# Kernel tuning notes

Measured on AMD Instinct MI355X. Metric: run time of the kernel, lower is better.

## Reference

```python
import jax, jax.numpy as jnp
import numpy as np
import math

DIM = 512
HEADS = 8
DH = DIM // HEADS
B, C, H, W = 2, 512, 48, 48


def setup_inputs() -> dict:
    key = jax.random.key(0)
    k1, k2, k3, k4 = jax.random.split(key, 4)
    x = jax.random.normal(k1, (B, C, H, W), dtype=jnp.float32)
    # torch Linear weights: [out_features, in_features]
    w_qkv = jax.random.normal(k2, (3 * DIM, DIM), dtype=jnp.float32) * (DIM ** -0.5)
    w_out = jax.random.normal(k3, (DIM, DIM), dtype=jnp.float32) * (DIM ** -0.5)
    b_out = jax.random.normal(k4, (DIM,), dtype=jnp.float32) * 0.01
    wavelength = jnp.asarray(0.1, dtype=jnp.float32)
    return {"x": x, "w_qkv": w_qkv, "w_out": w_out, "b_out": b_out, "wavelength": wavelength}


def reference(x, w_qkv, w_out, b_out, wavelength):
    b, c, h, w = x.shape
    n = h * w
    scale = DH ** -0.5

    x_flat = x.reshape(b, c, n).transpose(0, 2, 1)  # [B, N, C]
    qkv = jnp.einsum('bnc,dc->bnd', x_flat, w_qkv)   # [B, N, 3*DIM]
    q, k, v = jnp.split(qkv, 3, axis=-1)

    def to_heads(t):
        return t.reshape(b, n, HEADS, DH).transpose(0, 2, 1, 3)  # [B, h, N, dh]

    q, k, v = to_heads(q), to_heads(k), to_heads(v)

    dots = jnp.einsum('bhid,bhjd->bhij', q, k) * scale  # [B, h, N, N]

    # Fresnel interference bias over spatial positions
    yy, xx = jnp.meshgrid(jnp.arange(h), jnp.arange(w), indexing='ij')
    positions = jnp.stack([yy, xx], axis=-1).astype(jnp.float32).reshape(-1, 2)  # [N, 2]
    pos_diff = positions[None, :, :] - positions[:, None, :]  # [N, N, 2]
    distances = jnp.sqrt(jnp.sum(pos_diff ** 2, axis=-1) + 1e-8)  # [N, N]
    phase = 2.0 * math.pi * distances / (jnp.abs(wavelength) * h + 1e-6)
    interference = jnp.cos(phase)

    dots = dots + interference[None, None, :, :] * 0.1
    attn = jax.nn.softmax(dots, axis=-1)
    out = jnp.einsum('bhij,bhjd->bhid', attn, v)  # [B, h, N, dh]
    out = out.transpose(0, 2, 1, 3).reshape(b, n, HEADS * DH)  # [B, N, DIM]
    out = jnp.einsum('bnd,od->bno', out, w_out) + b_out
    return out.transpose(0, 2, 1).reshape(b, c, h, w)
```

## Files before the change

### kernel.cpp

```cpp
#include <hip/hip_runtime.h>
#include <math.h>

#define BB 2
#define CC 512
#define NN 2304
#define NH 8
#define DD 512
#define D3 1536
#define WIDTH 48
#define C1 0.18033688f

typedef _Float16 h8 __attribute__((ext_vector_type(8)));
typedef _Float16 h4 __attribute__((ext_vector_type(4)));
typedef _Float16 h2 __attribute__((ext_vector_type(2)));
typedef float f4 __attribute__((ext_vector_type(4)));

__device__ __forceinline__ void gload16(const void* g, void* s) {
  __builtin_amdgcn_global_load_lds(
      (const __attribute__((address_space(1))) unsigned int*)g,
      (__attribute__((address_space(3))) unsigned int*)s, 16, 0, 0);
}

__global__ __launch_bounds__(128) void btf_k(const float* __restrict__ wavp,
                                             _Float16* __restrict__ btf)
{
  const int t = threadIdx.x;
  const int qbk = blockIdx.x, ktk = blockIdx.y;
  const int w = t >> 6, quad = (t >> 4) & 3, l15 = t & 15;
  const float pc = 6.283185307179586f / (fabsf(wavp[0]) * (float)WIDTH + 1e-6f);
  _Float16* o = btf + (((size_t)qbk * 36 + ktk) * 128 + t) * 32;
#pragma unroll
  for (int g = 0; g < 4; ++g) {
    h8 v;
#pragma unroll
    for (int e = 0; e < 8; ++e) {
      const int j = g * 8 + e;
      const int nt = j >> 4, mt = (j >> 2) & 3, r = j & 3;
      const int q = qbk * 64 + w * 32 + nt * 16 + l15;
      const int k = ktk * 64 + mt * 16 + quad * 4 + r;
      const float dy = (float)(q / WIDTH) - (float)(k / WIDTH);
      const float dx = (float)(q % WIDTH) - (float)(k % WIDTH);
      const float dist = sqrtf(dy * dy + dx * dx + 1e-8f);
      v[e] = (_Float16)(0.1f * __cosf(dist * pc) * 1.44269504f);
    }
    *(h8*)(o + g * 8) = v;
  }
}

__global__ __launch_bounds__(256) void tx_k(const float* __restrict__ x,
                                            _Float16* __restrict__ xt)
{
  __shared__ float Ls[32][33];
  const int t = threadIdx.x;
  const int n0 = blockIdx.x * 32, c0 = blockIdx.y * 32, b = blockIdx.z;
#pragma unroll
  for (int p = 0; p < 4; ++p) {
    const int cl = (t >> 5) + p * 8, nl = t & 31;
    Ls[cl][nl] = x[((size_t)b * CC + c0 + cl) * NN + n0 + nl];
  }
  __syncthreads();
#pragma unroll
  for (int p = 0; p < 2; ++p) {
    const int nl = (t >> 4) + p * 16, cl = (t & 15) * 2;
    h2 v = {(_Float16)Ls[cl][nl], (_Float16)Ls[cl + 1][nl]};
    *(h2*)(xt + ((size_t)b * NN + n0 + nl) * CC + c0 + cl) = v;
  }
}

__global__ __launch_bounds__(256) void convw_k(const float* __restrict__ wq,
                                               const float* __restrict__ wo,
                                               _Float16* __restrict__ wqh,
                                               _Float16* __restrict__ woh)
{
  const int idx = blockIdx.x * 256 + threadIdx.x;
  const int NQ = (D3 * CC) / 4;
  if (idx < NQ) {
    float4 v = *(const float4*)(wq + (size_t)idx * 4);
    h4 o = {(_Float16)v.x, (_Float16)v.y, (_Float16)v.z, (_Float16)v.w};
    *(h4*)(wqh + (size_t)idx * 4) = o;
  } else {
    const int j = idx - NQ;
    float4 v = *(const float4*)(wo + (size_t)j * 4);
    h4 o = {(_Float16)v.x, (_Float16)v.y, (_Float16)v.z, (_Float16)v.w};
    *(h4*)(woh + (size_t)j * 4) = o;
  }
}

__global__ __launch_bounds__(64) void qkv_gemm_k(
    const _Float16* __restrict__ xt, const _Float16* __restrict__ wqh,
    _Float16* __restrict__ qb, _Float16* __restrict__ kb,
    _Float16* __restrict__ vb)
{
  __shared__ _Float16 Xs[2][64][32];
  __shared__ _Float16 Ws[2][64][32];
  const int t = threadIdx.x;
  const int l15 = t & 15, quad = t >> 4;
  const int n0 = blockIdx.x * 64;
  const int d0 = blockIdx.y * 64;
  const int b  = blockIdx.z;
  const bool isv = (d0 >= 2 * DD);
  const _Float16* xb = xt + (size_t)b * NN * CC;
  const int srow = t >> 2, scol = (t & 3) * 8;

  f4 acc[4][4];
#pragma unroll
  for (int mt = 0; mt < 4; ++mt)
#pragma unroll
    for (int nt = 0; nt < 4; ++nt) acc[mt][nt] = (f4)(0.f);

  auto stage = [&](int bf, int c0) {
#pragma unroll
    for (int ci = 0; ci < 4; ++ci) {
      const int row = ci * 16 + srow;
      gload16(xb + (size_t)(n0 + row) * CC + c0 + scol,
              &Xs[bf][0][0] + ci * 512);
      gload16(wqh + (size_t)(d0 + row) * CC + c0 + scol,
              &Ws[bf][0][0] + ci * 512);
    }
  };

  stage(0, 0);
  for (int i = 0; i < 16; ++i) {
    const int cur = i & 1;
    __syncthreads();
    if (i < 15) stage(cur ^ 1, (i + 1) * 32);
    h8 wfr[4], xfr[4];
#pragma unroll
    for (int mt = 0; mt < 4; ++mt)
      wfr[mt] = *(const h8*)&Ws[cur][mt * 16 + l15][quad * 8];
#pragma unroll
    for (int nt = 0; nt < 4; ++nt)
      xfr[nt] = *(const h8*)&Xs[cur][nt * 16 + l15][quad * 8];
    if (!isv) {
#pragma unroll
      for (int mt = 0; mt < 4; ++mt)
#pragma unroll
        for (int nt = 0; nt < 4; ++nt)
          acc[mt][nt] = __builtin_amdgcn_mfma_f32_16x16x32_f16(
              wfr[mt], xfr[nt], acc[mt][nt], 0, 0, 0);
    } else {
#pragma unroll
      for (int mt = 0; mt < 4; ++mt)
#pragma unroll
        for (int nt = 0; nt < 4; ++nt)
          acc[mt][nt] = __builtin_amdgcn_mfma_f32_16x16x32_f16(
              xfr[nt], wfr[mt], acc[mt][nt], 0, 0, 0);
    }
  }

  if (!isv) {
    const int which = d0 >> 9;
    _Float16* buf = which == 0 ? qb : kb;
    const int h = (d0 & 511) >> 6;
#pragma unroll
    for (int mt = 0; mt < 4; ++mt) {
      const int dh = mt * 16 + quad * 4;
#pragma unroll
      for (int nt = 0; nt < 4; ++nt) {
        const int token = n0 + nt * 16 + l15;
        h4 o = {(_Float16)acc[mt][nt][0], (_Float16)acc[mt][nt][1],
                (_Float16)acc[mt][nt][2], (_Float16)acc[mt][nt][3]};
        *(h4*)(buf + (((size_t)b * NH + h) * NN + token) * 64 + dh) = o;
      }
    }
  } else {
    const int h = (d0 - 2 * DD) >> 6;
#pragma unroll
    for (int mt = 0; mt < 4; ++mt) {
      const int dh = mt * 16 + l15;
#pragma unroll
      for (int nt = 0; nt < 4; ++nt) {
        const int token = n0 + nt * 16 + quad * 4;
        h4 o = {(_Float16)acc[mt][nt][0], (_Float16)acc[mt][nt][1],
                (_Float16)acc[mt][nt][2], (_Float16)acc[mt][nt][3]};
        *(h4*)(vb + (((size_t)b * NH + h) * 64 + dh) * NN + token) = o;
      }
    }
  }
}

__global__ __launch_bounds__(128, 3) void attn_k(
    const _Float16* __restrict__ qb, const _Float16* __restrict__ kb,
    const _Float16* __restrict__ vb, const _Float16* __restrict__ btf,
    _Float16* __restrict__ op, float* __restrict__ lp)
{
  __shared__ _Float16 Ks[64][72];
  __shared__ _Float16 Vs[64][72];
  __shared__ _Float16 Ps[2][32][72];

  const int t    = threadIdx.x;
  const int lane = t & 63;
  const int w    = t >> 6;
  const int l15  = lane & 15;
  const int quad = lane >> 4;
  const int qt = blockIdx.x >> 1;
  const int s  = blockIdx.x & 1;
  const int h = blockIdx.y, b = blockIdx.z;
  const int n0 = qt * 64;
  const size_t base = ((size_t)b * NH + h) * NN * 64;
  const _Float16* qp = qb + base;
  const _Float16* kp = kb + base;
  const _Float16* vp = vb + base;

  h8 qf[2][2];
#pragma unroll
  for (int nt = 0; nt < 2; ++nt)
#pragma unroll
    for (int ks = 0; ks < 2; ++ks)
      qf[nt][ks] = *(const h8*)(qp + (size_t)(n0 + w * 32 + nt * 16 + l15) * 64 +
                                ks * 32 + quad * 8);

  f4 oc[4][2];
#pragma unroll
  for (int mt = 0; mt < 4; ++mt)
#pragma unroll
    for (int nt = 0; nt < 2; ++nt) oc[mt][nt] = (f4)(0.f);
  float lacc[2][4] = {};

  const int srow = t >> 3, soff = (t & 7) * 8;
  const _Float16* bp = btf + (((size_t)qt * 36 + s * 18) * 128 + t) * 32;

  h8 kr[4], vr[4], br[4];
  {
    const int k0 = s * 18 * 64;
#pragma unroll
    for (int r = 0; r < 4; ++r) {
      const int row = srow + r * 16;
      kr[r] = *(const h8*)(kp + (size_t)(k0 + row) * 64 + soff);
      vr[r] = *(const h8*)(vp + (size_t)row * NN + k0 + soff);
      br[r] = *(const h8*)(bp + r * 8);
    }
  }

  for (int kt = 0; kt < 18; ++kt) {
    __syncthreads();
#pragma unroll
    for (int r = 0; r < 4; ++r) {
      const int row = srow + r * 16;
      *(h8*)&Ks[row][soff] = kr[r];
      *(h8*)&Vs[row][soff] = vr[r];
    }
    h8 bfr[4];
#pragma unroll
    for (int r = 0; r < 4; ++r) bfr[r] = br[r];
    __syncthreads();

    if (kt < 17) {
      const int k0n = (s * 18 + kt + 1) * 64;
      bp += 128 * 32;
#pragma unroll
      for (int r = 0; r < 4; ++r) {
        const int row = srow + r * 16;
        kr[r] = *(const h8*)(kp + (size_t)(k0n + row) * 64 + soff);
        vr[r] = *(const h8*)(vp + (size_t)row * NN + k0n + soff);
        br[r] = *(const h8*)(bp + r * 8);
      }
    }

    f4 st[4][2];
#pragma unroll
    for (int mt = 0; mt < 4; ++mt)
#pragma unroll
      for (int nt = 0; nt < 2; ++nt) st[mt][nt] = (f4)(0.f);
#pragma unroll
    for (int ks = 0; ks < 2; ++ks)
#pragma unroll
      for (int mt = 0; mt < 4; ++mt) {
        h8 kf = *(const h8*)&Ks[mt * 16 + l15][ks * 32 + quad * 8];
#pragma unroll
        for (int nt = 0; nt < 2; ++nt)
          st[mt][nt] = __builtin_amdgcn_mfma_f32_16x16x32_f16(
              kf, qf[nt][ks], st[mt][nt], 0, 0, 0);
      }

#pragma unroll
    for (int nt = 0; nt < 2; ++nt) {
      const int q = nt * 16 + l15;
#pragma unroll
      for (int mt = 0; mt < 4; ++mt) {
        h4 pk;
#pragma unroll
        for (int r = 0; r < 4; ++r) {
          const int j = nt * 16 + mt * 4 + r;
          const float bias = (float)bfr[j >> 3][j & 7];
          const float p = __builtin_exp2f(st[mt][nt][r] * C1 + bias);
          lacc[nt][r] += p;
          pk[r] = (_Float16)p;
        }
        *(h4*)&Ps[w][q][mt * 16 + quad * 4] = pk;
      }
    }

#pragma unroll
    for (int ks = 0; ks < 2; ++ks) {
      h8 pf[2];
#pragma unroll
      for (int nt = 0; nt < 2; ++nt)
        pf[nt] = *(const h8*)&Ps[w][nt * 16 + l15][ks * 32 + quad * 8];
#pragma unroll
      for (int mt = 0; mt < 4; ++mt) {
        h8 vf = *(const h8*)&Vs[mt * 16 + l15][ks * 32 + quad * 8];
#pragma unroll
        for (int nt = 0; nt < 2; ++nt)
          oc[mt][nt] = __builtin_amdgcn_mfma_f32_16x16x32_f16(
              vf, pf[nt], oc[mt][nt], 0, 0, 0);
      }
    }
  }

#pragma unroll
  for (int nt = 0; nt < 2; ++nt) {
    float l = lacc[nt][0] + lacc[nt][1] + lacc[nt][2] + lacc[nt][3];
    l += __shfl_xor(l, 16);
    l += __shfl_xor(l, 32);
    const float inv = 1.f / l;
    const int qi = n0 + w * 32 + nt * 16 + l15;
    _Float16* od = op + (size_t)s * BB * NN * DD +
                   ((size_t)b * NN + qi) * DD + h * 64;
#pragma unroll
    for (int mt = 0; mt < 4; ++mt) {
      const int dh = mt * 16 + quad * 4;
      h4 o = {(_Float16)(oc[mt][nt][0] * inv), (_Float16)(oc[mt][nt][1] * inv),
              (_Float16)(oc[mt][nt][2] * inv), (_Float16)(oc[mt][nt][3] * inv)};
      *(h4*)(od + dh) = o;
    }
    if (quad == 0)
      lp[(size_t)s * BB * NH * NN + ((size_t)b * NH + h) * NN + qi] = l;
  }
}

__global__ __launch_bounds__(256) void comb_k(
    const _Float16* __restrict__ op, const float* __restrict__ lp,
    _Float16* __restrict__ ho)
{
  const int idx = blockIdx.x * 256 + threadIdx.x;
  const int d8 = idx & 63;
  const int bn = idx >> 6;
  const int n = bn % NN, b = bn / NN;
  const int h = d8 >> 3;
  const float l0 = lp[((size_t)b * NH + h) * NN + n];
  const float l1 = lp[(size_t)BB * NH * NN + ((size_t)b * NH + h) * NN + n];
  const float inv = 1.f / (l0 + l1);
  const float w0 = l0 * inv, w1 = l1 * inv;
  h8 o0 = *(const h8*)(op + (size_t)bn * DD + d8 * 8);
  h8 o1 = *(const h8*)(op + (size_t)BB * NN * DD + (size_t)bn * DD + d8 * 8);
  h8 r;
#pragma unroll
  for (int i = 0; i < 8; ++i)
    r[i] = (_Float16)((float)o0[i] * w0 + (float)o1[i] * w1);
  *(h8*)(ho + (size_t)bn * DD + d8 * 8) = r;
}

__global__ __launch_bounds__(64) void out_gemm_k(
    const _Float16* __restrict__ ho, const _Float16* __restrict__ woh,
    const float* __restrict__ bias, float* __restrict__ out)
{
  __shared__ _Float16 Hs[2][64][32];
  __shared__ _Float16 Ws2[2][64][32];
  const int t = threadIdx.x;
  const int l15 = t & 15, quad = t >> 4;
  const int n0 = blockIdx.x * 64;
  const int o0 = blockIdx.y * 64;
  const int b  = blockIdx.z;
  const int srow = t >> 2, scol = (t & 3) * 8;

  f4 acc[4][4];
#pragma unroll
  for (int mt = 0; mt < 4; ++mt)
#pragma unroll
    for (int nt = 0; nt < 4; ++nt) acc[mt][nt] = (f4)(0.f);

  auto stage = [&](int bf, int c0) {
#pragma unroll
    for (int ci = 0; ci < 4; ++ci) {
      const int row = ci * 16 + srow;
      gload16(ho + ((size_t)b * NN + n0 + row) * DD + c0 + scol,
              &Hs[bf][0][0] + ci * 512);
      gload16(woh + (size_t)(o0 + row) * DD + c0 + scol,
              &Ws2[bf][0][0] + ci * 512);
    }
  };

  stage(0, 0);
  for (int i = 0; i < 16; ++i) {
    const int cur = i & 1;
    __syncthreads();
    if (i < 15) stage(cur ^ 1, (i + 1) * 32);
    h8 hf[4], wf[4];
#pragma unroll
    for (int mt = 0; mt < 4; ++mt)
      hf[mt] = *(const h8*)&Hs[cur][mt * 16 + l15][quad * 8];
#pragma unroll
    for (int nt = 0; nt < 4; ++nt)
      wf[nt] = *(const h8*)&Ws2[cur][nt * 16 + l15][quad * 8];
#pragma unroll
    for (int mt = 0; mt < 4; ++mt)
#pragma unroll
      for (int nt = 0; nt < 4; ++nt)
        acc[mt][nt] = __builtin_amdgcn_mfma_f32_16x16x32_f16(
            hf[mt], wf[nt], acc[mt][nt], 0, 0, 0);
  }

#pragma unroll
  for (int nt = 0; nt < 4; ++nt) {
    const int o = o0 + nt * 16 + l15;
    const float bv = bias[o];
#pragma unroll
    for (int mt = 0; mt < 4; ++mt) {
      const int token = n0 + mt * 16 + quad * 4;
      float4 v = {acc[mt][nt][0] + bv, acc[mt][nt][1] + bv,
                  acc[mt][nt][2] + bv, acc[mt][nt][3] + bv};
      *(float4*)(out + ((size_t)b * DD + o) * NN + token) = v;
    }
  }
}

extern "C" void kernel_launch(void* const* d_in, const int* in_sizes, int n_in,
                              void* d_out, int out_size, void* d_ws, size_t ws_size,
                              hipStream_t stream)
{
  (void)in_sizes; (void)n_in; (void)out_size; (void)ws_size;
  const float* x     = (const float*)d_in[0];
  const float* w_qkv = (const float*)d_in[1];
  const float* w_out = (const float*)d_in[2];
  const float* b_out = (const float*)d_in[3];
  const float* wav   = (const float*)d_in[4];
  float* out = (float*)d_out;

  const size_t SZ  = (size_t)BB * NH * NN * 64;
  const size_t BTF = (size_t)36 * 36 * 128 * 32;

  _Float16* qb  = (_Float16*)d_ws;
  _Float16* kb  = qb + SZ;
  _Float16* vb  = kb + SZ;
  _Float16* btf = vb + SZ;
  _Float16* op  = btf + BTF;
  float*    lpf = (float*)(op + 2 * SZ);
  _Float16* woh = (_Float16*)(lpf + 2 * (size_t)BB * NH * NN);
  _Float16* ho  = btf;
  _Float16* xt  = op;
  _Float16* wqh = op + SZ;

  btf_k     <<<dim3(36, 36), 128, 0, stream>>>(wav, btf);
  tx_k      <<<dim3(NN / 32, CC / 32, BB), 256, 0, stream>>>(x, xt);
  convw_k   <<<dim3((D3 * CC + DD * DD) / 1024), 256, 0, stream>>>(w_qkv, w_out, wqh, woh);
  qkv_gemm_k<<<dim3(NN / 64, D3 / 64, BB), 64, 0, stream>>>(xt, wqh, qb, kb, vb);
  attn_k    <<<dim3(NN / 64 * 2, NH, BB), 128, 0, stream>>>(qb, kb, vb, btf, op, lpf);
  comb_k    <<<dim3((BB * NN * 64) / 256), 256, 0, stream>>>(op, lpf, ho);
  out_gemm_k<<<dim3(NN / 64, DD / 64, BB), 64, 0, stream>>>(ho, woh, b_out, out);
}
```

Baseline: 177.1 us.

## Split attention keys four ways with atomic fp32 accumulation and fuse combine into output GEMM

```diff
diff --git a/kernel.cpp b/kernel.cpp
--- a/kernel.cpp
+++ b/kernel.cpp
@@ -9,6 +9,8 @@
 #define D3 1536
 #define WIDTH 48
 #define C1 0.18033688f
+#define NSPLIT 4
+#define KTILES 9
 
 typedef _Float16 h8 __attribute__((ext_vector_type(8)));
 typedef _Float16 h4 __attribute__((ext_vector_type(4)));
@@ -21,68 +23,70 @@
       (__attribute__((address_space(3))) unsigned int*)s, 16, 0, 0);
 }
 
-__global__ __launch_bounds__(128) void btf_k(const float* __restrict__ wavp,
-                                             _Float16* __restrict__ btf)
-{
-  const int t = threadIdx.x;
-  const int qbk = blockIdx.x, ktk = blockIdx.y;
-  const int w = t >> 6, quad = (t >> 4) & 3, l15 = t & 15;
-  const float pc = 6.283185307179586f / (fabsf(wavp[0]) * (float)WIDTH + 1e-6f);
-  _Float16* o = btf + (((size_t)qbk * 36 + ktk) * 128 + t) * 32;
-#pragma unroll
-  for (int g = 0; g < 4; ++g) {
-    h8 v;
-#pragma unroll
-    for (int e = 0; e < 8; ++e) {
-      const int j = g * 8 + e;
-      const int nt = j >> 4, mt = (j >> 2) & 3, r = j & 3;
-      const int q = qbk * 64 + w * 32 + nt * 16 + l15;
-      const int k = ktk * 64 + mt * 16 + quad * 4 + r;
-      const float dy = (float)(q / WIDTH) - (float)(k / WIDTH);
-      const float dx = (float)(q % WIDTH) - (float)(k % WIDTH);
-      const float dist = sqrtf(dy * dy + dx * dx + 1e-8f);
-      v[e] = (_Float16)(0.1f * __cosf(dist * pc) * 1.44269504f);
-    }
-    *(h8*)(o + g * 8) = v;
-  }
-}
-
-__global__ __launch_bounds__(256) void tx_k(const float* __restrict__ x,
-                                            _Float16* __restrict__ xt)
+__global__ __launch_bounds__(256) void prep_k(
+    const float* __restrict__ x, const float* __restrict__ wq,
+    const float* __restrict__ wo, const float* __restrict__ wavp,
+    _Float16* __restrict__ btf, _Float16* __restrict__ xt,
+    _Float16* __restrict__ wqh, _Float16* __restrict__ woh)
 {
   __shared__ float Ls[32][33];
   const int t = threadIdx.x;
-  const int n0 = blockIdx.x * 32, c0 = blockIdx.y * 32, b = blockIdx.z;
-#pragma unroll
-  for (int p = 0; p < 4; ++p) {
-    const int cl = (t >> 5) + p * 8, nl = t & 31;
-    Ls[cl][nl] = x[((size_t)b * CC + c0 + cl) * NN + n0 + nl];
-  }
-  __syncthreads();
-#pragma unroll
-  for (int p = 0; p < 2; ++p) {
-    const int nl = (t >> 4) + p * 16, cl = (t & 15) * 2;
-    h2 v = {(_Float16)Ls[cl][nl], (_Float16)Ls[cl + 1][nl]};
-    *(h2*)(xt + ((size_t)b * NN + n0 + nl) * CC + c0 + cl) = v;
-  }
-}
-
-__global__ __launch_bounds__(256) void convw_k(const float* __restrict__ wq,
-                                               const float* __restrict__ wo,
-                                               _Float16* __restrict__ wqh,
-                                               _Float16* __restrict__ woh)
-{
-  const int idx = blockIdx.x * 256 + threadIdx.x;
-  const int NQ = (D3 * CC) / 4;
-  if (idx < NQ) {
-    float4 v = *(const float4*)(wq + (size_t)idx * 4);
-    h4 o = {(_Float16)v.x, (_Float16)v.y, (_Float16)v.z, (_Float16)v.w};
-    *(h4*)(wqh + (size_t)idx * 4) = o;
+  const int bx = blockIdx.x;
+  const int job = blockIdx.y;
+
+  if (job == 0) {
+    if (bx >= 648) return;
+    const int gid = bx * 256 + t;
+    const int tile = gid >> 7, tid = gid & 127;
+    const int qbk = tile / 36, ktk = tile % 36;
+    const int w = tid >> 6, quad = (tid >> 4) & 3, l15 = tid & 15;
+    const float pc = 6.283185307179586f / (fabsf(wavp[0]) * (float)WIDTH + 1e-6f);
+    _Float16* o = btf + (((size_t)qbk * 36 + ktk) * 128 + tid) * 32;
+#pragma unroll
+    for (int g = 0; g < 4; ++g) {
+      h8 v;
+#pragma unroll
+      for (int e = 0; e < 8; ++e) {
+        const int j = g * 8 + e;
+        const int nt = j >> 4, mt = (j >> 2) & 3, r = j & 3;
+        const int q = qbk * 64 + w * 32 + nt * 16 + l15;
+        const int k = ktk * 64 + mt * 16 + quad * 4 + r;
+        const float dy = (float)(q / WIDTH) - (float)(k / WIDTH);
+        const float dx = (float)(q % WIDTH) - (float)(k % WIDTH);
+        const float dist = sqrtf(dy * dy + dx * dx + 1e-8f);
+        v[e] = (_Float16)(0.1f * __cosf(dist * pc) * 1.44269504f);
+      }
+      *(h8*)(o + g * 8) = v;
+    }
+  } else if (job == 1) {
+    const int b = bx / 1152, rem = bx % 1152;
+    const int c0 = (rem / 72) * 32, n0 = (rem % 72) * 32;
+#pragma unroll
+    for (int p = 0; p < 4; ++p) {
+      const int cl = (t >> 5) + p * 8, nl = t & 31;
+      Ls[cl][nl] = x[((size_t)b * CC + c0 + cl) * NN + n0 + nl];
+    }
+    __syncthreads();
+#pragma unroll
+    for (int p = 0; p < 2; ++p) {
+      const int nl = (t >> 4) + p * 16, cl = (t & 15) * 2;
+      h2 v = {(_Float16)Ls[cl][nl], (_Float16)Ls[cl + 1][nl]};
+      *(h2*)(xt + ((size_t)b * NN + n0 + nl) * CC + c0 + cl) = v;
+    }
   } else {
-    const int j = idx - NQ;
-    float4 v = *(const float4*)(wo + (size_t)j * 4);
-    h4 o = {(_Float16)v.x, (_Float16)v.y, (_Float16)v.z, (_Float16)v.w};
-    *(h4*)(woh + (size_t)j * 4) = o;
+    if (bx >= 1024) return;
+    const int idx = bx * 256 + t;
+    const int NQ = (D3 * CC) / 4;
+    if (idx < NQ) {
+      float4 v = *(const float4*)(wq + (size_t)idx * 4);
+      h4 o = {(_Float16)v.x, (_Float16)v.y, (_Float16)v.z, (_Float16)v.w};
+      *(h4*)(wqh + (size_t)idx * 4) = o;
+    } else {
+      const int j = idx - NQ;
+      float4 v = *(const float4*)(wo + (size_t)j * 4);
+      h4 o = {(_Float16)v.x, (_Float16)v.y, (_Float16)v.z, (_Float16)v.w};
+      *(h4*)(woh + (size_t)j * 4) = o;
+    }
   }
 }
 
@@ -182,7 +186,7 @@
 __global__ __launch_bounds__(128, 3) void attn_k(
     const _Float16* __restrict__ qb, const _Float16* __restrict__ kb,
     const _Float16* __restrict__ vb, const _Float16* __restrict__ btf,
-    _Float16* __restrict__ op, float* __restrict__ lp)
+    float* __restrict__ Oacc, float* __restrict__ lsum)
 {
   __shared__ _Float16 Ks[64][72];
   __shared__ _Float16 Vs[64][72];
@@ -193,8 +197,8 @@
   const int w    = t >> 6;
   const int l15  = lane & 15;
   const int quad = lane >> 4;
-  const int qt = blockIdx.x >> 1;
-  const int s  = blockIdx.x & 1;
+  const int qt = blockIdx.x >> 2;
+  const int s  = blockIdx.x & 3;
   const int h = blockIdx.y, b = blockIdx.z;
   const int n0 = qt * 64;
   const size_t base = ((size_t)b * NH + h) * NN * 64;
@@ -218,11 +222,11 @@
   float lacc[2][4] = {};
 
   const int srow = t >> 3, soff = (t & 7) * 8;
-  const _Float16* bp = btf + (((size_t)qt * 36 + s * 18) * 128 + t) * 32;
-
-  h8 kr[4], vr[4], br[4];
-  {
-    const int k0 = s * 18 * 64;
+  const _Float16* bp = btf + (((size_t)qt * 36 + s * KTILES) * 128 + t) * 32;
+
+  for (int kt = 0; kt < KTILES; ++kt) {
+    const int k0 = (s * KTILES + kt) * 64;
+    h8 kr[4], vr[4], br[4];
 #pragma unroll
     for (int r = 0; r < 4; ++r) {
       const int row = srow + r * 16;
@@ -230,9 +234,7 @@
       vr[r] = *(const h8*)(vp + (size_t)row * NN + k0 + soff);
       br[r] = *(const h8*)(bp + r * 8);
     }
-  }
-
-  for (int kt = 0; kt < 18; ++kt) {
+    bp += 128 * 32;
     __syncthreads();
 #pragma unroll
     for (int r = 0; r < 4; ++r) {
@@ -240,22 +242,7 @@
       *(h8*)&Ks[row][soff] = kr[r];
       *(h8*)&Vs[row][soff] = vr[r];
     }
-    h8 bfr[4];
-#pragma unroll
-    for (int r = 0; r < 4; ++r) bfr[r] = br[r];
     __syncthreads();
-
-    if (kt < 17) {
-      const int k0n = (s * 18 + kt + 1) * 64;
-      bp += 128 * 32;
-#pragma unroll
-      for (int r = 0; r < 4; ++r) {
-        const int row = srow + r * 16;
-        kr[r] = *(const h8*)(kp + (size_t)(k0n + row) * 64 + soff);
-        vr[r] = *(const h8*)(vp + (size_t)row * NN + k0n + soff);
-        br[r] = *(const h8*)(bp + r * 8);
-      }
-    }
 
     f4 st[4][2];
 #pragma unroll
@@ -282,7 +269,7 @@
 #pragma unroll
         for (int r = 0; r < 4; ++r) {
           const int j = nt * 16 + mt * 4 + r;
-          const float bias = (float)bfr[j >> 3][j & 7];
+          const float bias = (float)br[j >> 3][j & 7];
           const float p = __builtin_exp2f(st[mt][nt][r] * C1 + bias);
           lacc[nt][r] += p;
           pk[r] = (_Float16)p;
@@ -313,49 +300,24 @@
     float l = lacc[nt][0] + lacc[nt][1] + lacc[nt][2] + lacc[nt][3];
     l += __shfl_xor(l, 16);
     l += __shfl_xor(l, 32);
-    const float inv = 1.f / l;
     const int qi = n0 + w * 32 + nt * 16 + l15;
-    _Float16* od = op + (size_t)s * BB * NN * DD +
-                   ((size_t)b * NN + qi) * DD + h * 64;
-#pragma unroll
-    for (int mt = 0; mt < 4; ++mt) {
-      const int dh = mt * 16 + quad * 4;
-      h4 o = {(_Float16)(oc[mt][nt][0] * inv), (_Float16)(oc[mt][nt][1] * inv),
-              (_Float16)(oc[mt][nt][2] * inv), (_Float16)(oc[mt][nt][3] * inv)};
-      *(h4*)(od + dh) = o;
-    }
+    float* od = Oacc + ((size_t)b * NN + qi) * DD + h * 64;
+#pragma unroll
+    for (int mt = 0; mt < 4; ++mt)
+#pragma unroll
+      for (int r = 0; r < 4; ++r)
+        atomicAdd(od + mt * 16 + quad * 4 + r, oc[mt][nt][r]);
     if (quad == 0)
-      lp[(size_t)s * BB * NH * NN + ((size_t)b * NH + h) * NN + qi] = l;
-  }
-}
-
-__global__ __launch_bounds__(256) void comb_k(
-    const _Float16* __restrict__ op, const float* __restrict__ lp,
-    _Float16* __restrict__ ho)
+      atomicAdd(lsum + ((size_t)b * NH + h) * NN + qi, l);
+  }
+}
+
+__global__ __launch_bounds__(64) void outcomb_k(
+    const float* __restrict__ Oacc, const float* __restrict__ lsum,
+    const _Float16* __restrict__ woh, const float* __restrict__ bias,
+    float* __restrict__ out)
 {
-  const int idx = blockIdx.x * 256 + threadIdx.x;
-  const int d8 = idx & 63;
-  const int bn = idx >> 6;
-  const int n = bn % NN, b = bn / NN;
-  const int h = d8 >> 3;
-  const float l0 = lp[((size_t)b * NH + h) * NN + n];
-  const float l1 = lp[(size_t)BB * NH * NN + ((size_t)b * NH + h) * NN + n];
-  const float inv = 1.f / (l0 + l1);
-  const float w0 = l0 * inv, w1 = l1 * inv;
-  h8 o0 = *(const h8*)(op + (size_t)bn * DD + d8 * 8);
-  h8 o1 = *(const h8*)(op + (size_t)BB * NN * DD + (size_t)bn * DD + d8 * 8);
-  h8 r;
-#pragma unroll
-  for (int i = 0; i < 8; ++i)
-    r[i] = (_Float16)((float)o0[i] * w0 + (float)o1[i] * w1);
-  *(h8*)(ho + (size_t)bn * DD + d8 * 8) = r;
-}
-
-__global__ __launch_bounds__(64) void out_gemm_k(
-    const _Float16* __restrict__ ho, const _Float16* __restrict__ woh,
-    const float* __restrict__ bias, float* __restrict__ out)
-{
-  __shared__ _Float16 Hs[2][64][32];
+  __shared__ _Float16 Hs[64][32];
   __shared__ _Float16 Ws2[2][64][32];
   const int t = threadIdx.x;
   const int l15 = t & 15, quad = t >> 4;
@@ -370,26 +332,49 @@
 #pragma unroll
     for (int nt = 0; nt < 4; ++nt) acc[mt][nt] = (f4)(0.f);
 
-  auto stage = [&](int bf, int c0) {
+  auto stage_w = [&](int bf, int c0) {
+#pragma unroll
+    for (int ci = 0; ci < 4; ++ci)
+      gload16(woh + (size_t)(o0 + ci * 16 + srow) * DD + c0 + scol,
+              &Ws2[bf][0][0] + ci * 512);
+  };
+
+  float4 orow[4][2];
+  float invr[4];
+  auto load_o = [&](int c0) {
+    const int h = c0 >> 6;
 #pragma unroll
     for (int ci = 0; ci < 4; ++ci) {
-      const int row = ci * 16 + srow;
-      gload16(ho + ((size_t)b * NN + n0 + row) * DD + c0 + scol,
-              &Hs[bf][0][0] + ci * 512);
-      gload16(woh + (size_t)(o0 + row) * DD + c0 + scol,
-              &Ws2[bf][0][0] + ci * 512);
+      const int row = n0 + ci * 16 + srow;
+      const float* p = Oacc + ((size_t)b * NN + row) * DD + c0 + scol;
+      orow[ci][0] = *(const float4*)p;
+      orow[ci][1] = *(const float4*)(p + 4);
+      invr[ci] = 1.f / lsum[((size_t)b * NH + h) * NN + row];
     }
   };
 
-  stage(0, 0);
+  stage_w(0, 0);
+  load_o(0);
   for (int i = 0; i < 16; ++i) {
     const int cur = i & 1;
     __syncthreads();
-    if (i < 15) stage(cur ^ 1, (i + 1) * 32);
+#pragma unroll
+    for (int ci = 0; ci < 4; ++ci) {
+      const float iv = invr[ci];
+      h8 v = {(_Float16)(orow[ci][0].x * iv), (_Float16)(orow[ci][0].y * iv),
+              (_Float16)(orow[ci][0].z * iv), (_Float16)(orow[ci][0].w * iv),
+              (_Float16)(orow[ci][1].x * iv), (_Float16)(orow[ci][1].y * iv),
+              (_Float16)(orow[ci][1].z * iv), (_Float16)(orow[ci][1].w * iv)};
+      *(h8*)&Hs[ci * 16 + srow][scol] = v;
+    }
+    if (i < 15) {
+      stage_w(cur ^ 1, (i + 1) * 32);
+      load_o((i + 1) * 32);
+    }
     h8 hf[4], wf[4];
 #pragma unroll
     for (int mt = 0; mt < 4; ++mt)
-      hf[mt] = *(const h8*)&Hs[cur][mt * 16 + l15][quad * 8];
+      hf[mt] = *(const h8*)&Hs[mt * 16 + l15][quad * 8];
 #pragma unroll
     for (int nt = 0; nt < 4; ++nt)
       wf[nt] = *(const h8*)&Ws2[cur][nt * 16 + l15][quad * 8];
@@ -434,18 +419,20 @@
   _Float16* kb  = qb + SZ;
   _Float16* vb  = kb + SZ;
   _Float16* btf = vb + SZ;
-  _Float16* op  = btf + BTF;
-  float*    lpf = (float*)(op + 2 * SZ);
-  _Float16* woh = (_Float16*)(lpf + 2 * (size_t)BB * NH * NN);
-  _Float16* ho  = btf;
-  _Float16* xt  = op;
-  _Float16* wqh = op + SZ;
-
-  btf_k     <<<dim3(36, 36), 128, 0, stream>>>(wav, btf);
-  tx_k      <<<dim3(NN / 32, CC / 32, BB), 256, 0, stream>>>(x, xt);
-  convw_k   <<<dim3((D3 * CC + DD * DD) / 1024), 256, 0, stream>>>(w_qkv, w_out, wqh, woh);
+  float* Oacc   = (float*)(btf + BTF);
+  float* lsm    = Oacc + (size_t)BB * NN * DD;
+  _Float16* woh = (_Float16*)(lsm + (size_t)BB * NH * NN);
+  _Float16* xt  = (_Float16*)Oacc;
+  _Float16* wqh = xt + SZ;
+
+  prep_k    <<<dim3(2304, 3), 256, 0, stream>>>(x, w_qkv, w_out, wav,
+                                                btf, xt, wqh, woh);
   qkv_gemm_k<<<dim3(NN / 64, D3 / 64, BB), 64, 0, stream>>>(xt, wqh, qb, kb, vb);
-  attn_k    <<<dim3(NN / 64 * 2, NH, BB), 128, 0, stream>>>(qb, kb, vb, btf, op, lpf);
-  comb_k    <<<dim3((BB * NN * 64) / 256), 256, 0, stream>>>(op, lpf, ho);
-  out_gemm_k<<<dim3(NN / 64, DD / 64, BB), 64, 0, stream>>>(ho, woh, b_out, out);
-}
+  hipMemsetAsync(Oacc, 0,
+                 ((size_t)BB * NN * DD + (size_t)BB * NH * NN) * sizeof(float),
+                 stream);
+  attn_k    <<<dim3(NN / 64 * NSPLIT, NH, BB), 128, 0, stream>>>(
+                 qb, kb, vb, btf, Oacc, lsm);
+  outcomb_k <<<dim3(NN / 64, DD / 64, BB), 64, 0, stream>>>(
+                 Oacc, lsm, woh, b_out, out);
+}
```

Measured after the change: 269.2 us. 52.0% more time.
